# Performance work log

Measured on AMD Instinct MI355X. Metric: run time of the kernel, lower is better.

The kernel has to match this reference:

```python
import jax, jax.numpy as jnp
import numpy as np

N, IN_F, OUT_F = 8192, 512, 256
NEG_INF = -9e15
LEAKY_SLOPE = 0.25


def setup_inputs() -> dict:
    key = jax.random.key(0)
    k1, k2, k3, k4, k5, k6 = jax.random.split(key, 6)
    inp = {
        "input": jax.random.normal(k1, (N, IN_F), dtype=jnp.float32),
        "adj": jax.random.randint(k2, (N, N), 0, 2, dtype=jnp.int32),
        # learned params (xavier-normal-ish scale)
        "weights": jax.random.normal(k3, (IN_F, OUT_F), dtype=jnp.float32) * (2.0 / (IN_F + OUT_F)) ** 0.5,
        "a1": jax.random.normal(k4, (OUT_F, 1), dtype=jnp.float32) * (2.0 / (OUT_F + 1)) ** 0.5,
        "a2": jax.random.normal(k5, (OUT_F, 1), dtype=jnp.float32) * (2.0 / (OUT_F + 1)) ** 0.5,
        "bias": jax.random.uniform(k6, (OUT_F,), dtype=jnp.float32, minval=-1.0 / OUT_F ** 0.5, maxval=1.0 / OUT_F ** 0.5),
    }
    return inp


def reference(input, adj, weights, a1, a2, bias):
    # h = input @ W  : [N, out]
    h = input @ weights
    # e[i,j] = leaky_relu((h@a1)[i] + (h@a2)[j])  : [N, N] via broadcast
    e1 = h @ a1  # [N,1]
    e2 = h @ a2  # [N,1]
    e = e1 + e2.T
    e = jnp.where(e > 0, e, LEAKY_SLOPE * e)
    # mask non-edges, row softmax (dropout omitted: deterministic reference)
    scores = jnp.where(adj > 0, e, NEG_INF)
    attention = jax.nn.softmax(scores, axis=1)
    # aggregate + bias
    return attention @ h + bias
```

## Files before the change

kernel.cpp:

```cpp
#include <hip/hip_runtime.h>

typedef __attribute__((ext_vector_type(8))) short short8;
typedef __attribute__((ext_vector_type(4))) float floatx4;
typedef __attribute__((ext_vector_type(4))) unsigned int uintx4;
typedef __attribute__((ext_vector_type(2))) unsigned int uintx2;
typedef __attribute__((ext_vector_type(4))) int intx4;
typedef __attribute__((ext_vector_type(4))) unsigned short ushortx4;

#define NN 8192
#define KIN 512
#define COUT 256
#define SHIFT 16.0f

__device__ __forceinline__ unsigned int f2bf(float f) {
  unsigned int u = __float_as_uint(f);
  return (u + 0x7FFFu + ((u >> 16) & 1u)) >> 16;
}

__device__ __forceinline__ short8 pack8(const float* p) {
  uintx4 w;
  w.x = f2bf(p[0]) | (f2bf(p[1]) << 16);
  w.y = f2bf(p[2]) | (f2bf(p[3]) << 16);
  w.z = f2bf(p[4]) | (f2bf(p[5]) << 16);
  w.w = f2bf(p[6]) | (f2bf(p[7]) << 16);
  union { uintx4 u; short8 s; } cv; cv.u = w;
  return cv.s;
}

__global__ void k_cast_input(const float* __restrict__ in, ushortx4* __restrict__ out) {
  int idx = blockIdx.x * 256 + threadIdx.x;
  floatx4 v = ((const floatx4*)in)[idx];
  ushortx4 o;
  o.x = (unsigned short)f2bf(v.x);
  o.y = (unsigned short)f2bf(v.y);
  o.z = (unsigned short)f2bf(v.z);
  o.w = (unsigned short)f2bf(v.w);
  out[idx] = o;
}

__global__ void k_prep_w(const float* __restrict__ w, unsigned short* __restrict__ wt) {
  int idx = blockIdx.x * 256 + threadIdx.x;
  int k = idx >> 8, c = idx & 255;
  wt[c * KIN + k] = (unsigned short)f2bf(w[idx]);
}

__global__ __launch_bounds__(256)
void k_gemm_h(const unsigned short* __restrict__ inA, const unsigned short* __restrict__ wt,
              const float* __restrict__ a1, const float* __restrict__ a2,
              unsigned short* __restrict__ ht, float* __restrict__ e1, float* __restrict__ e2) {
  int wave = threadIdx.x >> 6;
  int lane = threadIdx.x & 63;
  int n = lane & 15, q = lane >> 4;
  int row0 = blockIdx.x * 64 + wave * 16;
  int mrow = row0 + n;

  floatx4 acc[16];
#pragma unroll
  for (int t = 0; t < 16; ++t) acc[t] = (floatx4){0.f, 0.f, 0.f, 0.f};

  for (int kc = 0; kc < KIN / 32; ++kc) {
    int k0 = kc * 32 + q * 8;
    short8 a = *(const short8*)(inA + (size_t)mrow * KIN + k0);
#pragma unroll
    for (int nt = 0; nt < 16; ++nt) {
      short8 b = *(const short8*)(wt + (size_t)(nt * 16 + n) * KIN + k0);
      acc[nt] = __builtin_amdgcn_mfma_f32_16x16x32_bf16(a, b, acc[nt], 0, 0, 0);
    }
  }

  int i0 = row0 + q * 4;
#pragma unroll
  for (int nt = 0; nt < 16; ++nt) {
    int c = nt * 16 + n;
    uintx2 pk;
    pk.x = f2bf(acc[nt][0]) | (f2bf(acc[nt][1]) << 16);
    pk.y = f2bf(acc[nt][2]) | (f2bf(acc[nt][3]) << 16);
    *(uintx2*)(ht + (size_t)c * NN + i0) = pk;
  }

  float s1[4] = {0.f, 0.f, 0.f, 0.f}, s2[4] = {0.f, 0.f, 0.f, 0.f};
#pragma unroll
  for (int nt = 0; nt < 16; ++nt) {
    float w1 = a1[nt * 16 + n];
    float w2 = a2[nt * 16 + n];
#pragma unroll
    for (int r = 0; r < 4; ++r) {
      s1[r] += acc[nt][r] * w1;
      s2[r] += acc[nt][r] * w2;
    }
  }
#pragma unroll
  for (int m = 1; m < 16; m <<= 1) {
#pragma unroll
    for (int r = 0; r < 4; ++r) {
      s1[r] += __shfl_xor(s1[r], m);
      s2[r] += __shfl_xor(s2[r], m);
    }
  }
  if (n == 0) {
#pragma unroll
    for (int r = 0; r < 4; ++r) {
      e1[i0 + r] = s1[r];
      e2[i0 + r] = s2[r];
    }
  }
}

__global__ __launch_bounds__(256, 2)
void k_attn_part(const int* __restrict__ adj, const unsigned short* __restrict__ ht,
                 const float* __restrict__ e1, const float* __restrict__ e2,
                 float* __restrict__ opart, float* __restrict__ Dpart) {
  int b = blockIdx.x;
  int rg = b >> 3, js = b & 7;
  int wave = threadIdx.x >> 6, lane = threadIdx.x & 63;
  int n = lane & 15, q = lane >> 4;
  int rowbase = rg * 128 + wave * 32;

  float e1v0 = e1[rowbase + n];
  float e1v1 = e1[rowbase + 16 + n];

  const int* rowp0 = adj + (size_t)(rowbase + n) * NN;
  const int* rowp1 = adj + (size_t)(rowbase + 16 + n) * NN;

  floatx4 acc[2][16];
#pragma unroll
  for (int t = 0; t < 2; ++t)
#pragma unroll
    for (int nt = 0; nt < 16; ++nt) acc[t][nt] = (floatx4){0.f, 0.f, 0.f, 0.f};

  float d0 = 0.f, d1 = 0.f;
  int jbeg = js * 1024;

  int jp = jbeg + q * 8;
  intx4 A00 = *(const intx4*)(rowp0 + jp);
  intx4 A01 = *(const intx4*)(rowp0 + jp + 4);
  intx4 A10 = *(const intx4*)(rowp1 + jp);
  intx4 A11 = *(const intx4*)(rowp1 + jp + 4);

  for (int ch = 0; ch < 32; ++ch) {
    int j0 = jbeg + ch * 32 + q * 8;
    int jn = jbeg + (((ch + 1) & 31) * 32) + q * 8;
    intx4 B00 = *(const intx4*)(rowp0 + jn);
    intx4 B01 = *(const intx4*)(rowp0 + jn + 4);
    intx4 B10 = *(const intx4*)(rowp1 + jn);
    intx4 B11 = *(const intx4*)(rowp1 + jn + 4);

    floatx4 ea = *(const floatx4*)(e2 + j0);
    floatx4 eb = *(const floatx4*)(e2 + j0 + 4);
    float ev[8] = {ea.x, ea.y, ea.z, ea.w, eb.x, eb.y, eb.z, eb.w};

    float p0[8], p1[8];
#pragma unroll
    for (int jj = 0; jj < 8; ++jj) {
      int av0 = (jj < 4) ? A00[jj] : A01[jj - 4];
      int av1 = (jj < 4) ? A10[jj] : A11[jj - 4];
      float t0 = e1v0 + ev[jj];
      float t1 = e1v1 + ev[jj];
      float f0 = fmaxf(t0, 0.25f * t0);
      float f1 = fmaxf(t1, 0.25f * t1);
      float x0 = __expf(f0 - SHIFT);
      float x1 = __expf(f1 - SHIFT);
      p0[jj] = (av0 != 0) ? x0 : 0.f;
      p1[jj] = (av1 != 0) ? x1 : 0.f;
      d0 += p0[jj];
      d1 += p1[jj];
    }
    short8 af0 = pack8(p0);
    short8 af1 = pack8(p1);

#pragma unroll
    for (int g = 0; g < 2; ++g) {
      short8 bf[8];
#pragma unroll
      for (int t = 0; t < 8; ++t)
        bf[t] = *(const short8*)(ht + (size_t)((g * 8 + t) * 16 + n) * NN + j0);
#pragma unroll
      for (int t = 0; t < 8; ++t) {
        acc[0][g * 8 + t] = __builtin_amdgcn_mfma_f32_16x16x32_bf16(af0, bf[t], acc[0][g * 8 + t], 0, 0, 0);
        acc[1][g * 8 + t] = __builtin_amdgcn_mfma_f32_16x16x32_bf16(af1, bf[t], acc[1][g * 8 + t], 0, 0, 0);
      }
    }

    A00 = B00; A01 = B01; A10 = B10; A11 = B11;
  }

  d0 += __shfl_xor(d0, 16); d0 += __shfl_xor(d0, 32);
  d1 += __shfl_xor(d1, 16); d1 += __shfl_xor(d1, 32);
  if (lane < 16) {
    Dpart[(size_t)js * NN + rowbase + lane] = d0;
    Dpart[(size_t)js * NN + rowbase + 16 + lane] = d1;
  }

  float* op = opart + (size_t)js * NN * COUT;
#pragma unroll
  for (int t2 = 0; t2 < 2; ++t2) {
#pragma unroll
    for (int nt = 0; nt < 16; ++nt) {
#pragma unroll
      for (int r = 0; r < 4; ++r) {
        int i = rowbase + t2 * 16 + q * 4 + r;
        op[(size_t)i * COUT + nt * 16 + n] = acc[t2][nt][r];
      }
    }
  }
}

__global__ void k_final_part(float* __restrict__ out, const float* __restrict__ opart,
                             const float* __restrict__ Dpart, const float* __restrict__ bias) {
  int i = blockIdx.x;
  int c = threadIdx.x;
  float s = 0.f, d = 0.f;
#pragma unroll
  for (int js = 0; js < 8; ++js) {
    s += opart[((size_t)js * NN + i) * COUT + c];
    d += Dpart[(size_t)js * NN + i];
  }
  out[(size_t)i * COUT + c] = s / fmaxf(d, 1e-37f) + bias[c];
}

__global__ __launch_bounds__(256, 2)
void k_attn_atomic(const int* __restrict__ adj, const unsigned short* __restrict__ ht,
                   const float* __restrict__ e1, const float* __restrict__ e2,
                   float* __restrict__ out_num, float* __restrict__ Dbuf) {
  int b = blockIdx.x;
  int rg = b >> 3, js = b & 7;
  int wave = threadIdx.x >> 6, lane = threadIdx.x & 63;
  int n = lane & 15, q = lane >> 4;
  int rowbase = rg * 128 + wave * 32;

  float e1v0 = e1[rowbase + n];
  float e1v1 = e1[rowbase + 16 + n];

  floatx4 acc[2][16];
#pragma unroll
  for (int t = 0; t < 2; ++t)
#pragma unroll
    for (int nt = 0; nt < 16; ++nt) acc[t][nt] = (floatx4){0.f, 0.f, 0.f, 0.f};

  float d0 = 0.f, d1 = 0.f;
  int jbeg = js * 1024;

  for (int ch = 0; ch < 32; ++ch) {
    int j0 = jbeg + ch * 32 + q * 8;
    floatx4 ea = *(const floatx4*)(e2 + j0);
    floatx4 eb = *(const floatx4*)(e2 + j0 + 4);
    float ev[8] = {ea.x, ea.y, ea.z, ea.w, eb.x, eb.y, eb.z, eb.w};

    intx4 A00 = *(const intx4*)(adj + (size_t)(rowbase + n) * NN + j0);
    intx4 A01 = *(const intx4*)(adj + (size_t)(rowbase + n) * NN + j0 + 4);
    intx4 A10 = *(const intx4*)(adj + (size_t)(rowbase + 16 + n) * NN + j0);
    intx4 A11 = *(const intx4*)(adj + (size_t)(rowbase + 16 + n) * NN + j0 + 4);

    float p0[8], p1[8];
#pragma unroll
    for (int jj = 0; jj < 8; ++jj) {
      int av0 = (jj < 4) ? A00[jj] : A01[jj - 4];
      int av1 = (jj < 4) ? A10[jj] : A11[jj - 4];
      float t0 = e1v0 + ev[jj];
      float t1 = e1v1 + ev[jj];
      float f0 = fmaxf(t0, 0.25f * t0);
      float f1 = fmaxf(t1, 0.25f * t1);
      float x0 = __expf(f0 - SHIFT);
      float x1 = __expf(f1 - SHIFT);
      p0[jj] = (av0 != 0) ? x0 : 0.f;
      p1[jj] = (av1 != 0) ? x1 : 0.f;
      d0 += p0[jj];
      d1 += p1[jj];
    }
    short8 af0 = pack8(p0);
    short8 af1 = pack8(p1);

#pragma unroll
    for (int g = 0; g < 2; ++g) {
      short8 bf[8];
#pragma unroll
      for (int t = 0; t < 8; ++t)
        bf[t] = *(const short8*)(ht + (size_t)((g * 8 + t) * 16 + n) * NN + j0);
#pragma unroll
      for (int t = 0; t < 8; ++t) {
        acc[0][g * 8 + t] = __builtin_amdgcn_mfma_f32_16x16x32_bf16(af0, bf[t], acc[0][g * 8 + t], 0, 0, 0);
        acc[1][g * 8 + t] = __builtin_amdgcn_mfma_f32_16x16x32_bf16(af1, bf[t], acc[1][g * 8 + t], 0, 0, 0);
      }
    }
  }

  d0 += __shfl_xor(d0, 16); d0 += __shfl_xor(d0, 32);
  d1 += __shfl_xor(d1, 16); d1 += __shfl_xor(d1, 32);
  if (lane < 16) {
    atomicAdd(Dbuf + rowbase + lane, d0);
    atomicAdd(Dbuf + rowbase + 16 + lane, d1);
  }

#pragma unroll
  for (int t2 = 0; t2 < 2; ++t2) {
#pragma unroll
    for (int nt = 0; nt < 16; ++nt) {
#pragma unroll
      for (int r = 0; r < 4; ++r) {
        int i = rowbase + t2 * 16 + q * 4 + r;
        atomicAdd(out_num + (size_t)i * COUT + nt * 16 + n, acc[t2][nt][r]);
      }
    }
  }
}

__global__ void k_final_atomic(float* __restrict__ out, const float* __restrict__ Dbuf,
                               const float* __restrict__ bias) {
  int idx = blockIdx.x * 256 + threadIdx.x;
  int i = idx >> 8, c = idx & 255;
  float d = fmaxf(Dbuf[i], 1e-37f);
  out[idx] = out[idx] / d + bias[c];
}

extern "C" void kernel_launch(void* const* d_in, const int* in_sizes, int n_in,
                              void* d_out, int out_size, void* d_ws, size_t ws_size,
                              hipStream_t stream) {
  const float* input   = (const float*)d_in[0];
  const int*   adj     = (const int*)d_in[1];
  const float* weights = (const float*)d_in[2];
  const float* a1      = (const float*)d_in[3];
  const float* a2      = (const float*)d_in[4];
  const float* bias    = (const float*)d_in[5];
  float* out = (float*)d_out;
  char* ws = (char*)d_ws;

  unsigned short* inA = (unsigned short*)(ws);
  unsigned short* wt  = (unsigned short*)(ws + 8388608);
  unsigned short* ht  = (unsigned short*)(ws + 8650752);
  float* e1    = (float*)(ws + 12845056);
  float* e2    = (float*)(ws + 12877824);
  float* Dpart = (float*)(ws + 12910592);
  float* opart = (float*)(ws + 13172736);
  const size_t WS_NEEDED_PART = 13172736 + (size_t)8 * NN * COUT * 4;
  float* Dbuf = Dpart;

  k_cast_input<<<4096, 256, 0, stream>>>(input, (ushortx4*)inA);
  k_prep_w<<<512, 256, 0, stream>>>(weights, wt);
  k_gemm_h<<<128, 256, 0, stream>>>(inA, wt, a1, a2, ht, e1, e2);

  if (ws_size >= WS_NEEDED_PART) {
    k_attn_part<<<512, 256, 0, stream>>>(adj, ht, e1, e2, opart, Dpart);
    k_final_part<<<8192, 256, 0, stream>>>(out, opart, Dpart, bias);
  } else {
    hipMemsetAsync(out, 0, (size_t)NN * COUT * sizeof(float), stream);
    hipMemsetAsync(Dbuf, 0, NN * sizeof(float), stream);
    k_attn_atomic<<<512, 256, 0, stream>>>(adj, ht, e1, e2, out, Dbuf);
    k_final_atomic<<<8192, 256, 0, stream>>>(out, Dbuf, bias);
  }
}
```

Measured before the change: 533.4 us.

## Precompress adjacency matrix to bitmask before attention aggregation

Adds a pre-pass kernel that reads the int32 adjacency matrix in fully coalesced fashion and packs it into 32-bit bitmasks, 32 edges per word. The attention kernel then loads one small mask word per row per chunk instead of strided int32 vectors, which frees registers and load bandwidth inside the MFMA loop. The cost is an extra kernel launch, still one full read of the adjacency matrix, and 8 MB more workspace, which may force the atomic fallback path if the workspace is too small.

```diff
diff --git a/kernel.cpp b/kernel.cpp
--- a/kernel.cpp
+++ b/kernel.cpp
@@ -25,6 +25,22 @@
   w.w = f2bf(p[6]) | (f2bf(p[7]) << 16);
   union { uintx4 u; short8 s; } cv; cv.u = w;
   return cv.s;
+}
+
+__global__ __launch_bounds__(256)
+void k_compress(const int* __restrict__ adj, unsigned int* __restrict__ bm) {
+  int idx = blockIdx.x * 256 + threadIdx.x;
+  const int* p = adj + (size_t)idx * 32;
+  unsigned int m = 0;
+#pragma unroll
+  for (int k = 0; k < 8; ++k) {
+    intx4 v = *(const intx4*)(p + k * 4);
+    m |= (v.x != 0 ? 1u : 0u) << (k * 4 + 0);
+    m |= (v.y != 0 ? 1u : 0u) << (k * 4 + 1);
+    m |= (v.z != 0 ? 1u : 0u) << (k * 4 + 2);
+    m |= (v.w != 0 ? 1u : 0u) << (k * 4 + 3);
+  }
+  bm[idx] = m;
 }
 
 __global__ void k_cast_input(const float* __restrict__ in, ushortx4* __restrict__ out) {
@@ -107,7 +123,7 @@
 }
 
 __global__ __launch_bounds__(256, 2)
-void k_attn_part(const int* __restrict__ adj, const unsigned short* __restrict__ ht,
+void k_attn_part(const unsigned int* __restrict__ bm, const unsigned short* __restrict__ ht,
                  const float* __restrict__ e1, const float* __restrict__ e2,
                  float* __restrict__ opart, float* __restrict__ Dpart) {
   int b = blockIdx.x;
@@ -119,8 +135,8 @@
   float e1v0 = e1[rowbase + n];
   float e1v1 = e1[rowbase + 16 + n];
 
-  const int* rowp0 = adj + (size_t)(rowbase + n) * NN;
-  const int* rowp1 = adj + (size_t)(rowbase + 16 + n) * NN;
+  const unsigned int* bp0 = bm + (size_t)(rowbase + n) * 256 + js * 32;
+  const unsigned int* bp1 = bm + (size_t)(rowbase + 16 + n) * 256 + js * 32;
 
   floatx4 acc[2][16];
 #pragma unroll
@@ -131,23 +147,120 @@
   float d0 = 0.f, d1 = 0.f;
   int jbeg = js * 1024;
 
-  int jp = jbeg + q * 8;
-  intx4 A00 = *(const intx4*)(rowp0 + jp);
-  intx4 A01 = *(const intx4*)(rowp0 + jp + 4);
-  intx4 A10 = *(const intx4*)(rowp1 + jp);
-  intx4 A11 = *(const intx4*)(rowp1 + jp + 4);
+  unsigned int W0 = bp0[0];
+  unsigned int W1 = bp1[0];
 
   for (int ch = 0; ch < 32; ++ch) {
     int j0 = jbeg + ch * 32 + q * 8;
-    int jn = jbeg + (((ch + 1) & 31) * 32) + q * 8;
-    intx4 B00 = *(const intx4*)(rowp0 + jn);
-    intx4 B01 = *(const intx4*)(rowp0 + jn + 4);
-    intx4 B10 = *(const intx4*)(rowp1 + jn);
-    intx4 B11 = *(const intx4*)(rowp1 + jn + 4);
+    unsigned int NW0 = bp0[(ch + 1) & 31];
+    unsigned int NW1 = bp1[(ch + 1) & 31];
 
     floatx4 ea = *(const floatx4*)(e2 + j0);
     floatx4 eb = *(const floatx4*)(e2 + j0 + 4);
     float ev[8] = {ea.x, ea.y, ea.z, ea.w, eb.x, eb.y, eb.z, eb.w};
+
+    unsigned int by0 = (W0 >> (q * 8)) & 0xffu;
+    unsigned int by1 = (W1 >> (q * 8)) & 0xffu;
+
+    float p0[8], p1[8];
+#pragma unroll
+    for (int jj = 0; jj < 8; ++jj) {
+      float t0 = e1v0 + ev[jj];
+      float t1 = e1v1 + ev[jj];
+      float f0 = fmaxf(t0, 0.25f * t0);
+      float f1 = fmaxf(t1, 0.25f * t1);
+      float x0 = __expf(f0 - SHIFT);
+      float x1 = __expf(f1 - SHIFT);
+      p0[jj] = ((by0 >> jj) & 1u) ? x0 : 0.f;
+      p1[jj] = ((by1 >> jj) & 1u) ? x1 : 0.f;
+      d0 += p0[jj];
+      d1 += p1[jj];
+    }
+    short8 af0 = pack8(p0);
+    short8 af1 = pack8(p1);
+
+#pragma unroll
+    for (int g = 0; g < 2; ++g) {
+      short8 bf[8];
+#pragma unroll
+      for (int t = 0; t < 8; ++t)
+        bf[t] = *(const short8*)(ht + (size_t)((g * 8 + t) * 16 + n) * NN + j0);
+#pragma unroll
+      for (int t = 0; t < 8; ++t) {
+        acc[0][g * 8 + t] = __builtin_amdgcn_mfma_f32_16x16x32_bf16(af0, bf[t], acc[0][g * 8 + t], 0, 0, 0);
+        acc[1][g * 8 + t] = __builtin_amdgcn_mfma_f32_16x16x32_bf16(af1, bf[t], acc[1][g * 8 + t], 0, 0, 0);
+      }
+    }
+
+    W0 = NW0; W1 = NW1;
+  }
+
+  d0 += __shfl_xor(d0, 16); d0 += __shfl_xor(d0, 32);
+  d1 += __shfl_xor(d1, 16); d1 += __shfl_xor(d1, 32);
+  if (lane < 16) {
+    Dpart[(size_t)js * NN + rowbase + lane] = d0;
+    Dpart[(size_t)js * NN + rowbase + 16 + lane] = d1;
+  }
+
+  float* op = opart + (size_t)js * NN * COUT;
+#pragma unroll
+  for (int t2 = 0; t2 < 2; ++t2) {
+#pragma unroll
+    for (int nt = 0; nt < 16; ++nt) {
+#pragma unroll
+      for (int r = 0; r < 4; ++r) {
+        int i = rowbase + t2 * 16 + q * 4 + r;
+        op[(size_t)i * COUT + nt * 16 + n] = acc[t2][nt][r];
+      }
+    }
+  }
+}
+
+__global__ void k_final_part(float* __restrict__ out, const float* __restrict__ opart,
+                             const float* __restrict__ Dpart, const float* __restrict__ bias) {
+  int i = blockIdx.x;
+  int c = threadIdx.x;
+  float s = 0.f, d = 0.f;
+#pragma unroll
+  for (int js = 0; js < 8; ++js) {
+    s += opart[((size_t)js * NN + i) * COUT + c];
+    d += Dpart[(size_t)js * NN + i];
+  }
+  out[(size_t)i * COUT + c] = s / fmaxf(d, 1e-37f) + bias[c];
+}
+
+__global__ __launch_bounds__(256, 2)
+void k_attn_atomic(const int* __restrict__ adj, const unsigned short* __restrict__ ht,
+                   const float* __restrict__ e1, const float* __restrict__ e2,
+                   float* __restrict__ out_num, float* __restrict__ Dbuf) {
+  int b = blockIdx.x;
+  int rg = b >> 3, js = b & 7;
+  int wave = threadIdx.x >> 6, lane = threadIdx.x & 63;
+  int n = lane & 15, q = lane >> 4;
+  int rowbase = rg * 128 + wave * 32;
+
+  float e1v0 = e1[rowbase + n];
+  float e1v1 = e1[rowbase + 16 + n];
+
+  floatx4 acc[2][16];
+#pragma unroll
+  for (int t = 0; t < 2; ++t)
+#pragma unroll
+    for (int nt = 0; nt < 16; ++nt) acc[t][nt] = (floatx4){0.f, 0.f, 0.f, 0.f};
+
+  float d0 = 0.f, d1 = 0.f;
+  int jbeg = js * 1024;
+
+  for (int ch = 0; ch < 32; ++ch) {
+    int j0 = jbeg + ch * 32 + q * 8;
+    floatx4 ea = *(const floatx4*)(e2 + j0);
+    floatx4 eb = *(const floatx4*)(e2 + j0 + 4);
+    float ev[8] = {ea.x, ea.y, ea.z, ea.w, eb.x, eb.y, eb.z, eb.w};
+
+    intx4 A00 = *(const intx4*)(adj + (size_t)(rowbase + n) * NN + j0);
+    intx4 A01 = *(const intx4*)(adj + (size_t)(rowbase + n) * NN + j0 + 4);
+    intx4 A10 = *(const intx4*)(adj + (size_t)(rowbase + 16 + n) * NN + j0);
+    intx4 A11 = *(const intx4*)(adj + (size_t)(rowbase + 16 + n) * NN + j0 + 4);
 
     float p0[8], p1[8];
 #pragma unroll
@@ -180,108 +293,6 @@
         acc[1][g * 8 + t] = __builtin_amdgcn_mfma_f32_16x16x32_bf16(af1, bf[t], acc[1][g * 8 + t], 0, 0, 0);
       }
     }
-
-    A00 = B00; A01 = B01; A10 = B10; A11 = B11;
-  }
-
-  d0 += __shfl_xor(d0, 16); d0 += __shfl_xor(d0, 32);
-  d1 += __shfl_xor(d1, 16); d1 += __shfl_xor(d1, 32);
-  if (lane < 16) {
-    Dpart[(size_t)js * NN + rowbase + lane] = d0;
-    Dpart[(size_t)js * NN + rowbase + 16 + lane] = d1;
-  }
-
-  float* op = opart + (size_t)js * NN * COUT;
-#pragma unroll
-  for (int t2 = 0; t2 < 2; ++t2) {
-#pragma unroll
-    for (int nt = 0; nt < 16; ++nt) {
-#pragma unroll
-      for (int r = 0; r < 4; ++r) {
-        int i = rowbase + t2 * 16 + q * 4 + r;
-        op[(size_t)i * COUT + nt * 16 + n] = acc[t2][nt][r];
-      }
-    }
-  }
-}
-
-__global__ void k_final_part(float* __restrict__ out, const float* __restrict__ opart,
-                             const float* __restrict__ Dpart, const float* __restrict__ bias) {
-  int i = blockIdx.x;
-  int c = threadIdx.x;
-  float s = 0.f, d = 0.f;
-#pragma unroll
-  for (int js = 0; js < 8; ++js) {
-    s += opart[((size_t)js * NN + i) * COUT + c];
-    d += Dpart[(size_t)js * NN + i];
-  }
-  out[(size_t)i * COUT + c] = s / fmaxf(d, 1e-37f) + bias[c];
-}
-
-__global__ __launch_bounds__(256, 2)
-void k_attn_atomic(const int* __restrict__ adj, const unsigned short* __restrict__ ht,
-                   const float* __restrict__ e1, const float* __restrict__ e2,
-                   float* __restrict__ out_num, float* __restrict__ Dbuf) {
-  int b = blockIdx.x;
-  int rg = b >> 3, js = b & 7;
-  int wave = threadIdx.x >> 6, lane = threadIdx.x & 63;
-  int n = lane & 15, q = lane >> 4;
-  int rowbase = rg * 128 + wave * 32;
-
-  float e1v0 = e1[rowbase + n];
-  float e1v1 = e1[rowbase + 16 + n];
-
-  floatx4 acc[2][16];
-#pragma unroll
-  for (int t = 0; t < 2; ++t)
-#pragma unroll
-    for (int nt = 0; nt < 16; ++nt) acc[t][nt] = (floatx4){0.f, 0.f, 0.f, 0.f};
-
-  float d0 = 0.f, d1 = 0.f;
-  int jbeg = js * 1024;
-
-  for (int ch = 0; ch < 32; ++ch) {
-    int j0 = jbeg + ch * 32 + q * 8;
-    floatx4 ea = *(const floatx4*)(e2 + j0);
-    floatx4 eb = *(const floatx4*)(e2 + j0 + 4);
-    float ev[8] = {ea.x, ea.y, ea.z, ea.w, eb.x, eb.y, eb.z, eb.w};
-
-    intx4 A00 = *(const intx4*)(adj + (size_t)(rowbase + n) * NN + j0);
-    intx4 A01 = *(const intx4*)(adj + (size_t)(rowbase + n) * NN + j0 + 4);
-    intx4 A10 = *(const intx4*)(adj + (size_t)(rowbase + 16 + n) * NN + j0);
-    intx4 A11 = *(const intx4*)(adj + (size_t)(rowbase + 16 + n) * NN + j0 + 4);
-
-    float p0[8], p1[8];
-#pragma unroll
-    for (int jj = 0; jj < 8; ++jj) {
-      int av0 = (jj < 4) ? A00[jj] : A01[jj - 4];
-      int av1 = (jj < 4) ? A10[jj] : A11[jj - 4];
-      float t0 = e1v0 + ev[jj];
-      float t1 = e1v1 + ev[jj];
-      float f0 = fmaxf(t0, 0.25f * t0);
-      float f1 = fmaxf(t1, 0.25f * t1);
-      float x0 = __expf(f0 - SHIFT);
-      float x1 = __expf(f1 - SHIFT);
-      p0[jj] = (av0 != 0) ? x0 : 0.f;
-      p1[jj] = (av1 != 0) ? x1 : 0.f;
-      d0 += p0[jj];
-      d1 += p1[jj];
-    }
-    short8 af0 = pack8(p0);
-    short8 af1 = pack8(p1);
-
-#pragma unroll
-    for (int g = 0; g < 2; ++g) {
-      short8 bf[8];
-#pragma unroll
-      for (int t = 0; t < 8; ++t)
-        bf[t] = *(const short8*)(ht + (size_t)((g * 8 + t) * 16 + n) * NN + j0);
-#pragma unroll
-      for (int t = 0; t < 8; ++t) {
-        acc[0][g * 8 + t] = __builtin_amdgcn_mfma_f32_16x16x32_bf16(af0, bf[t], acc[0][g * 8 + t], 0, 0, 0);
-        acc[1][g * 8 + t] = __builtin_amdgcn_mfma_f32_16x16x32_bf16(af1, bf[t], acc[1][g * 8 + t], 0, 0, 0);
-      }
-    }
   }
 
   d0 += __shfl_xor(d0, 16); d0 += __shfl_xor(d0, 32);
@@ -330,18 +341,22 @@
   float* e1    = (float*)(ws + 12845056);
   float* e2    = (float*)(ws + 12877824);
   float* Dpart = (float*)(ws + 12910592);
-  float* opart = (float*)(ws + 13172736);
-  const size_t WS_NEEDED_PART = 13172736 + (size_t)8 * NN * COUT * 4;
+  unsigned int* bm = (unsigned int*)(ws + 13172736);
+  float* opart = (float*)(ws + 21561344);
+  const size_t WS_NEEDED_PART = 21561344 + (size_t)8 * NN * COUT * 4;
   float* Dbuf = Dpart;
 
-  k_cast_input<<<4096, 256, 0, stream>>>(input, (ushortx4*)inA);
-  k_prep_w<<<512, 256, 0, stream>>>(weights, wt);
-  k_gemm_h<<<128, 256, 0, stream>>>(inA, wt, a1, a2, ht, e1, e2);
-
   if (ws_size >= WS_NEEDED_PART) {
-    k_attn_part<<<512, 256, 0, stream>>>(adj, ht, e1, e2, opart, Dpart);
+    k_compress<<<8192, 256, 0, stream>>>(adj, bm);
+    k_cast_input<<<4096, 256, 0, stream>>>(input, (ushortx4*)inA);
+    k_prep_w<<<512, 256, 0, stream>>>(weights, wt);
+    k_gemm_h<<<128, 256, 0, stream>>>(inA, wt, a1, a2, ht, e1, e2);
+    k_attn_part<<<512, 256, 0, stream>>>(bm, ht, e1, e2, opart, Dpart);
     k_final_part<<<8192, 256, 0, stream>>>(out, opart, Dpart, bias);
   } else {
+    k_cast_input<<<4096, 256, 0, stream>>>(input, (ushortx4*)inA);
+    k_prep_w<<<512, 256, 0, stream>>>(weights, wt);
+    k_gemm_h<<<128, 256, 0, stream>>>(inA, wt, a1, a2, ht, e1, e2);
     hipMemsetAsync(out, 0, (size_t)NN * COUT * sizeof(float), stream);
     hipMemsetAsync(Dbuf, 0, NN * sizeof(float), stream);
     k_attn_atomic<<<512, 256, 0, stream>>>(adj, ht, e1, e2, out, Dbuf);
```

Result: slower. 567.3 us (+6.4%).
